# Kernel tuning notes

Hardware: AMD Instinct MI355X
Metric: run time of the kernel (lower is better)

Reference implementation:

```python
import jax, jax.numpy as jnp
import numpy as np

KERNEL_SIZE = 5
GROUP_SIZE = 1
SCALE = 2


def setup_inputs() -> dict:
    key = jax.random.key(0)
    k1, k2 = jax.random.split(key)
    N, C, H, W = 2, 256, 100, 100
    features = jax.random.normal(k1, (N, C, H, W), dtype=jnp.float32)
    masks = jax.random.uniform(
        k2, (N, KERNEL_SIZE * KERNEL_SIZE * GROUP_SIZE, H * SCALE, W * SCALE),
        dtype=jnp.float32)
    return {"features": features, "masks": masks}


def _carafe_naive(features, masks, k, g, s):
    N, C, H, W = features.shape
    r = (k - 1) // 2
    # zero-pad spatially, then gather the k*k neighborhood of every low-res pixel
    pad = jnp.pad(features, ((0, 0), (0, 0), (r, r), (r, r)))
    # patches: [N, C, k*k, H, W] -- fixed small loop over k*k shifts
    patches = jnp.stack(
        [pad[:, :, dy:dy + H, dx:dx + W] for dy in range(k) for dx in range(k)],
        axis=2)
    cg = C // g
    # masks: [N, g, k*k, H, s, W, s]  (output pixel (h*s+a, w*s+b))
    m = masks.reshape(N, g, k * k, H, s, W, s)
    # patches per group: [N, g, cg, k*k, H, W]
    p = patches.reshape(N, g, cg, k * k, H, W)
    # weighted sum over the k*k window; result [N, g, cg, H, s, W, s]
    out = jnp.einsum('ngkhawb,ngckhw->ngchawb', m, p)
    return out.reshape(N, C, H * s, W * s)


def reference(features, masks):
    return _carafe_naive(features, masks, KERNEL_SIZE, GROUP_SIZE, SCALE)
```

## Files before the change

kernel.cpp:

```cpp
#include <hip/hip_runtime.h>


#define N_ 2
#define C_ 256
#define H_ 100
#define W_ 100
#define CC 8
#define HW_ (H_ * W_)
#define OW_ (W_ * 2)
#define OHW_ (HW_ * 4)
#define NCHUNK (C_ / CC)
#define TH 10
#define TW 25
#define HY (TH + 4)
#define HX (TW + 4)
#define XP 32
#define TILES_X (W_ / TW)
#define TILES_Y (H_ / TH)

__global__ __launch_bounds__(256) void carafe_kernel(
    const float* __restrict__ feat,
    const float* __restrict__ mask,
    float* __restrict__ out) {

    __shared__ float lds[HY * 2 * XP * 4];

    const int tile = blockIdx.x;
    const int tx = tile % TILES_X;
    const int ty = tile / TILES_X;
    const int cchunk = blockIdx.y;
    const int n = blockIdx.z;
    const int x0 = tx * TW;
    const int y0 = ty * TH;
    const int t = threadIdx.x;

    const int lane = t & 31;
    const int g = t >> 5;
    const float* fbase = feat + (n * C_ + cchunk * CC) * HW_;

#pragma unroll
    for (int r = 0; r < 14; ++r) {
        const int p = r * 8 + g;
        const int c = p / HY;
        const int y = p % HY;
        const int yy = y0 - 2 + y;
        const int xx = x0 - 2 + lane;
        float v = 0.f;
        if (lane < HX && (unsigned)yy < (unsigned)H_ && (unsigned)xx < (unsigned)W_)
            v = fbase[c * HW_ + yy * W_ + xx];
        lds[((y * 2 + (c >> 2)) * XP + lane) * 4 + (c & 3)] = v;
    }
    __syncthreads();

    if (t >= TH * TW) return;
    const int hl = t / TW;
    const int wl = t % TW;

    float2 a0[CC], a1[CC];
#pragma unroll
    for (int c = 0; c < CC; ++c) {
        a0[c] = make_float2(0.f, 0.f);
        a1[c] = make_float2(0.f, 0.f);
    }

    const float4* lds4 = reinterpret_cast<const float4*>(lds);
    const int oh0 = 2 * (y0 + hl);
    const int ow0 = 2 * (x0 + wl);
    const float* mbase = mask + n * (25 * OHW_) + oh0 * OW_ + ow0;

#pragma unroll 2
    for (int dy = 0; dy < 5; ++dy) {
        const int yl = hl + dy;
#pragma unroll
        for (int dx = 0; dx < 5; ++dx) {
            const int tap = dy * 5 + dx;
            const float* mrow = mbase + tap * OHW_;
            const float2 m0 = *reinterpret_cast<const float2*>(mrow);
            const float2 m1 = *reinterpret_cast<const float2*>(mrow + OW_);

            const float4 lo = lds4[(yl * 2 + 0) * XP + (wl + dx)];
            const float4 hi = lds4[(yl * 2 + 1) * XP + (wl + dx)];
            const float f[8] = {lo.x, lo.y, lo.z, lo.w, hi.x, hi.y, hi.z, hi.w};

#pragma unroll
            for (int c = 0; c < CC; ++c) {
                a0[c].x = fmaf(f[c], m0.x, a0[c].x);
                a0[c].y = fmaf(f[c], m0.y, a0[c].y);
                a1[c].x = fmaf(f[c], m1.x, a1[c].x);
                a1[c].y = fmaf(f[c], m1.y, a1[c].y);
            }
        }
    }

    float* obase = out + (n * C_ + cchunk * CC) * OHW_ + oh0 * OW_ + ow0;
#pragma unroll
    for (int c = 0; c < CC; ++c) {
        *reinterpret_cast<float2*>(obase + c * OHW_) = a0[c];
        *reinterpret_cast<float2*>(obase + c * OHW_ + OW_) = a1[c];
    }
}

extern "C" void kernel_launch(void* const* d_in, const int* in_sizes, int n_in,
                              void* d_out, int out_size, void* d_ws, size_t ws_size,
                              hipStream_t stream) {
    const float* feat = (const float*)d_in[0];
    const float* mask = (const float*)d_in[1];
    float* out = (float*)d_out;

    dim3 grid(TILES_X * TILES_Y, NCHUNK, N_);
    carafe_kernel<<<grid, 256, 0, stream>>>(feat, mask, out);
}
```

Baseline: 45.25 us.

## Compute two adjacent low-res pixels per thread with register-cached LDS rows

Each thread now produces a 2x4 output patch covering two horizontally adjacent low-res pixels, loading six LDS feature vectors per row once and reusing them across the five dx taps and both pixels. Mask reads and output stores widen to float4. The tile changes to 20x25 with a padded LDS layout (every third slot skipped) to avoid bank conflicts, and the halo load is restructured to one channel per warp. Fewer threads per block are active (250 of 256) and register pressure rises from the doubled accumulators.

```diff
diff --git a/kernel.cpp b/kernel.cpp
--- a/kernel.cpp
+++ b/kernel.cpp
@@ -10,20 +10,21 @@
 #define OW_ (W_ * 2)
 #define OHW_ (HW_ * 4)
 #define NCHUNK (C_ / CC)
-#define TH 10
-#define TW 25
-#define HY (TH + 4)
-#define HX (TW + 4)
-#define XP 32
+#define TW 20
+#define TH 25
+#define HX 24
+#define HY 29
+#define PW 35
 #define TILES_X (W_ / TW)
 #define TILES_Y (H_ / TH)
+#define NPAIR (TW / 2)
 
 __global__ __launch_bounds__(256) void carafe_kernel(
     const float* __restrict__ feat,
     const float* __restrict__ mask,
     float* __restrict__ out) {
 
-    __shared__ float lds[HY * 2 * XP * 4];
+    __shared__ float lds[HY * 2 * PW * 4];
 
     const int tile = blockIdx.x;
     const int tx = tile % TILES_X;
@@ -37,57 +38,72 @@
     const int lane = t & 31;
     const int g = t >> 5;
     const float* fbase = feat + (n * C_ + cchunk * CC) * HW_;
-
+    {
+        const int plane = (g >> 2);
+        const int elem = (g & 3);
+        const int physx = lane + (lane >> 1);
+        const int xx = x0 - 2 + lane;
+        const bool xok = (lane < HX) & ((unsigned)xx < (unsigned)W_);
 #pragma unroll
-    for (int r = 0; r < 14; ++r) {
-        const int p = r * 8 + g;
-        const int c = p / HY;
-        const int y = p % HY;
-        const int yy = y0 - 2 + y;
-        const int xx = x0 - 2 + lane;
-        float v = 0.f;
-        if (lane < HX && (unsigned)yy < (unsigned)H_ && (unsigned)xx < (unsigned)W_)
-            v = fbase[c * HW_ + yy * W_ + xx];
-        lds[((y * 2 + (c >> 2)) * XP + lane) * 4 + (c & 3)] = v;
+        for (int r = 0; r < HY; ++r) {
+            const int yy = y0 - 2 + r;
+            float v = 0.f;
+            if (xok & ((unsigned)yy < (unsigned)H_))
+                v = fbase[g * HW_ + yy * W_ + xx];
+            if (lane < HX)
+                lds[((r * 2 + plane) * PW + physx) * 4 + elem] = v;
+        }
     }
     __syncthreads();
 
-    if (t >= TH * TW) return;
-    const int hl = t / TW;
-    const int wl = t % TW;
+    if (t >= NPAIR * TH) return;
+    const int hl = t / NPAIR;
+    const int wp = t % NPAIR;
 
-    float2 a0[CC], a1[CC];
+    float4 acc[CC][2];
 #pragma unroll
     for (int c = 0; c < CC; ++c) {
-        a0[c] = make_float2(0.f, 0.f);
-        a1[c] = make_float2(0.f, 0.f);
+        acc[c][0] = make_float4(0.f, 0.f, 0.f, 0.f);
+        acc[c][1] = make_float4(0.f, 0.f, 0.f, 0.f);
     }
 
     const float4* lds4 = reinterpret_cast<const float4*>(lds);
     const int oh0 = 2 * (y0 + hl);
-    const int ow0 = 2 * (x0 + wl);
+    const int ow0 = 2 * (x0 + 2 * wp);
     const float* mbase = mask + n * (25 * OHW_) + oh0 * OW_ + ow0;
 
-#pragma unroll 2
+    const int sw = 3 * wp;
+
+#pragma unroll 1
     for (int dy = 0; dy < 5; ++dy) {
-        const int yl = hl + dy;
+        const int rb0 = ((hl + dy) * 2 + 0) * PW + sw;
+        const int rb1 = rb0 + PW;
+
+        float4 fa[6], fb[6];
+#pragma unroll
+        for (int j = 0; j < 6; ++j) {
+            const int off = j + (j >> 1);
+            fa[j] = lds4[rb0 + off];
+            fb[j] = lds4[rb1 + off];
+        }
+
+        const float* mrow_dy = mbase + (dy * 5) * OHW_;
 #pragma unroll
         for (int dx = 0; dx < 5; ++dx) {
-            const int tap = dy * 5 + dx;
-            const float* mrow = mbase + tap * OHW_;
-            const float2 m0 = *reinterpret_cast<const float2*>(mrow);
-            const float2 m1 = *reinterpret_cast<const float2*>(mrow + OW_);
-
-            const float4 lo = lds4[(yl * 2 + 0) * XP + (wl + dx)];
-            const float4 hi = lds4[(yl * 2 + 1) * XP + (wl + dx)];
-            const float f[8] = {lo.x, lo.y, lo.z, lo.w, hi.x, hi.y, hi.z, hi.w};
-
+            const float4 m0 = *reinterpret_cast<const float4*>(mrow_dy + dx * OHW_);
+            const float4 m1 = *reinterpret_cast<const float4*>(mrow_dy + dx * OHW_ + OW_);
 #pragma unroll
             for (int c = 0; c < CC; ++c) {
-                a0[c].x = fmaf(f[c], m0.x, a0[c].x);
-                a0[c].y = fmaf(f[c], m0.y, a0[c].y);
-                a1[c].x = fmaf(f[c], m1.x, a1[c].x);
-                a1[c].y = fmaf(f[c], m1.y, a1[c].y);
+                const float fl = (c < 4) ? fa[dx][c] : fb[dx][c - 4];
+                const float fr = (c < 4) ? fa[dx + 1][c] : fb[dx + 1][c - 4];
+                acc[c][0].x = fmaf(fl, m0.x, acc[c][0].x);
+                acc[c][0].y = fmaf(fl, m0.y, acc[c][0].y);
+                acc[c][0].z = fmaf(fr, m0.z, acc[c][0].z);
+                acc[c][0].w = fmaf(fr, m0.w, acc[c][0].w);
+                acc[c][1].x = fmaf(fl, m1.x, acc[c][1].x);
+                acc[c][1].y = fmaf(fl, m1.y, acc[c][1].y);
+                acc[c][1].z = fmaf(fr, m1.z, acc[c][1].z);
+                acc[c][1].w = fmaf(fr, m1.w, acc[c][1].w);
             }
         }
     }
@@ -95,8 +111,8 @@
     float* obase = out + (n * C_ + cchunk * CC) * OHW_ + oh0 * OW_ + ow0;
 #pragma unroll
     for (int c = 0; c < CC; ++c) {
-        *reinterpret_cast<float2*>(obase + c * OHW_) = a0[c];
-        *reinterpret_cast<float2*>(obase + c * OHW_ + OW_) = a1[c];
+        *reinterpret_cast<float4*>(obase + c * OHW_) = acc[c][0];
+        *reinterpret_cast<float4*>(obase + c * OHW_ + OW_) = acc[c][1];
     }
 }
 
```

Result: slower. 52.73 us (+16.5%).

## Reorder grid for mask reuse, pack v2f FMAs, compact LDS layout

Applied to the files above, without the earlier changes.

The grid puts the channel chunk on x, so consecutive blocks share the same spatial tile and reuse its mask data from L2 instead of re-fetching it across chunks. The accumulation uses two-wide vector FMA builtins, aiming at packed FP32 FMA instructions. The feature load is rewritten so each thread loads four channels per row and stores them as one float4 into a compact LDS layout with an odd row stride of 29. Together these target mask bandwidth, FMA issue rate and LDS bank conflicts, with some added complexity in the indexing.

```diff
diff --git a/kernel.cpp b/kernel.cpp
--- a/kernel.cpp
+++ b/kernel.cpp
@@ -1,5 +1,7 @@
 #include <hip/hip_runtime.h>
 
+
+typedef float v2f __attribute__((ext_vector_type(2)));
 
 #define N_ 2
 #define C_ 256
@@ -10,45 +12,54 @@
 #define OW_ (W_ * 2)
 #define OHW_ (HW_ * 4)
 #define NCHUNK (C_ / CC)
+#define TW 25
 #define TH 10
-#define TW 25
-#define HY (TH + 4)
-#define HX (TW + 4)
-#define XP 32
+#define HX 29
+#define NROW 28
+#define RSTR 29
 #define TILES_X (W_ / TW)
 #define TILES_Y (H_ / TH)
+#define TILES (TILES_X * TILES_Y)
 
 __global__ __launch_bounds__(256) void carafe_kernel(
     const float* __restrict__ feat,
     const float* __restrict__ mask,
     float* __restrict__ out) {
 
-    __shared__ float lds[HY * 2 * XP * 4];
+    __shared__ float4 lds4[NROW * RSTR];
 
-    const int tile = blockIdx.x;
+    const int cchunk = blockIdx.x;
+    const int tile   = blockIdx.y;
+    const int n      = blockIdx.z;
     const int tx = tile % TILES_X;
     const int ty = tile / TILES_X;
-    const int cchunk = blockIdx.y;
-    const int n = blockIdx.z;
     const int x0 = tx * TW;
     const int y0 = ty * TH;
     const int t = threadIdx.x;
-
     const int lane = t & 31;
     const int g = t >> 5;
-    const float* fbase = feat + (n * C_ + cchunk * CC) * HW_;
 
+    {
+        const float* fb = feat + (n * C_ + cchunk * CC) * HW_;
+        const int xx = x0 - 2 + lane;
+        const bool xok = (lane < HX) & ((unsigned)xx < (unsigned)W_);
 #pragma unroll
-    for (int r = 0; r < 14; ++r) {
-        const int p = r * 8 + g;
-        const int c = p / HY;
-        const int y = p % HY;
-        const int yy = y0 - 2 + y;
-        const int xx = x0 - 2 + lane;
-        float v = 0.f;
-        if (lane < HX && (unsigned)yy < (unsigned)H_ && (unsigned)xx < (unsigned)W_)
-            v = fbase[c * HW_ + yy * W_ + xx];
-        lds[((y * 2 + (c >> 2)) * XP + lane) * 4 + (c & 3)] = v;
+        for (int r = 0; r < 4; ++r) {
+            const int p = g * 4 + r;
+            const int y = p >> 1;
+            const int cq = p & 1;
+            const int yy = y0 - 2 + y;
+            float v0 = 0.f, v1 = 0.f, v2 = 0.f, v3 = 0.f;
+            if (xok & ((unsigned)yy < (unsigned)H_) & (p < NROW)) {
+                const int o = (cq * 4) * HW_ + yy * W_ + xx;
+                v0 = fb[o];
+                v1 = fb[o + HW_];
+                v2 = fb[o + 2 * HW_];
+                v3 = fb[o + 3 * HW_];
+            }
+            if ((p < NROW) & (lane < HX))
+                lds4[p * RSTR + lane] = make_float4(v0, v1, v2, v3);
+        }
     }
     __syncthreads();
 
@@ -56,47 +67,39 @@
     const int hl = t / TW;
     const int wl = t % TW;
 
-    float2 a0[CC], a1[CC];
+    v2f a0[CC], a1[CC];
 #pragma unroll
-    for (int c = 0; c < CC; ++c) {
-        a0[c] = make_float2(0.f, 0.f);
-        a1[c] = make_float2(0.f, 0.f);
-    }
+    for (int c = 0; c < CC; ++c) { a0[c] = (v2f){0.f, 0.f}; a1[c] = (v2f){0.f, 0.f}; }
 
-    const float4* lds4 = reinterpret_cast<const float4*>(lds);
     const int oh0 = 2 * (y0 + hl);
     const int ow0 = 2 * (x0 + wl);
     const float* mbase = mask + n * (25 * OHW_) + oh0 * OW_ + ow0;
 
 #pragma unroll 2
     for (int dy = 0; dy < 5; ++dy) {
-        const int yl = hl + dy;
+        const int ry = (hl + dy) * 2;
+        const float* mrow_dy = mbase + (dy * 5) * OHW_;
 #pragma unroll
         for (int dx = 0; dx < 5; ++dx) {
-            const int tap = dy * 5 + dx;
-            const float* mrow = mbase + tap * OHW_;
-            const float2 m0 = *reinterpret_cast<const float2*>(mrow);
-            const float2 m1 = *reinterpret_cast<const float2*>(mrow + OW_);
-
-            const float4 lo = lds4[(yl * 2 + 0) * XP + (wl + dx)];
-            const float4 hi = lds4[(yl * 2 + 1) * XP + (wl + dx)];
+            const v2f m0 = *reinterpret_cast<const v2f*>(mrow_dy + dx * OHW_);
+            const v2f m1 = *reinterpret_cast<const v2f*>(mrow_dy + dx * OHW_ + OW_);
+            const float4 lo = lds4[ry * RSTR + wl + dx];
+            const float4 hi = lds4[(ry + 1) * RSTR + wl + dx];
             const float f[8] = {lo.x, lo.y, lo.z, lo.w, hi.x, hi.y, hi.z, hi.w};
-
 #pragma unroll
             for (int c = 0; c < CC; ++c) {
-                a0[c].x = fmaf(f[c], m0.x, a0[c].x);
-                a0[c].y = fmaf(f[c], m0.y, a0[c].y);
-                a1[c].x = fmaf(f[c], m1.x, a1[c].x);
-                a1[c].y = fmaf(f[c], m1.y, a1[c].y);
+                const v2f fv = {f[c], f[c]};
+                a0[c] = __builtin_elementwise_fma(fv, m0, a0[c]);
+                a1[c] = __builtin_elementwise_fma(fv, m1, a1[c]);
             }
         }
     }
 
-    float* obase = out + (n * C_ + cchunk * CC) * OHW_ + oh0 * OW_ + ow0;
+    float* ob = out + (n * C_ + cchunk * CC) * OHW_ + oh0 * OW_ + ow0;
 #pragma unroll
     for (int c = 0; c < CC; ++c) {
-        *reinterpret_cast<float2*>(obase + c * OHW_) = a0[c];
-        *reinterpret_cast<float2*>(obase + c * OHW_ + OW_) = a1[c];
+        *reinterpret_cast<v2f*>(ob + c * OHW_) = a0[c];
+        *reinterpret_cast<v2f*>(ob + c * OHW_ + OW_) = a1[c];
     }
 }
 
@@ -107,6 +110,6 @@
     const float* mask = (const float*)d_in[1];
     float* out = (float*)d_out;
 
-    dim3 grid(TILES_X * TILES_Y, NCHUNK, N_);
+    dim3 grid(NCHUNK, TILES, N_);
     carafe_kernel<<<grid, 256, 0, stream>>>(feat, mask, out);
 }
```

New measurement: 38.08 us. 1.19x faster.
